# Performance work log

Hardware: AMD Instinct MI355X
Metric: run time of the kernel (lower is better)

The kernel has to match this reference:

```python
import jax, jax.numpy as jnp
import numpy as np

N, M, C, CSKIP, K = 16384, 4096, 256, 128, 3
BIG = 1e10  # distance penalty for cross-batch pairs


def setup_inputs() -> dict:
    key = jax.random.key(0)
    ks = jax.random.split(key, 6)
    return {
        "x": jax.random.normal(ks[0], (M, C), jnp.float32),
        "pos": jax.random.normal(ks[1], (M, 3), jnp.float32),
        "batch": jnp.zeros((M,), jnp.int32),
        "x_skip": jax.random.normal(ks[2], (N, CSKIP), jnp.float32),
        "pos_skip": jax.random.normal(ks[3], (N, 3), jnp.float32),
        "batch_skip": jnp.zeros((N,), jnp.int32),
        "W1": jax.random.normal(ks[4], (C + CSKIP, 256), jnp.float32) * (1.0 / np.sqrt(C + CSKIP)),
        "b1": jnp.zeros((256,), jnp.float32),
        "W2": jax.random.normal(ks[5], (256, 256), jnp.float32) * (1.0 / np.sqrt(256)),
        "b2": jnp.zeros((256,), jnp.float32),
    }


def _knn_idx(pos, pos_skip, batch, batch_skip, k):
    # Squared distances via GEMM form: [N, M]
    a2 = jnp.sum(pos_skip * pos_skip, axis=-1, keepdims=True)      # [N,1]
    b2 = jnp.sum(pos * pos, axis=-1)[None, :]                       # [1,M]
    d2 = a2 + b2 - 2.0 * (pos_skip @ pos.T)                         # [N,M]
    d2 = jnp.where(batch_skip[:, None] != batch[None, :], BIG, d2)
    _, idx = jax.lax.top_k(-d2, k)                                  # [N,k]
    return idx


def reference(x, pos, batch, x_skip, pos_skip, batch_skip, W1, b1, W2, b2):
    idx = _knn_idx(pos, pos_skip, batch, batch_skip, K)             # [N,k] coarse neighbor ids
    # Exact squared dist recomputed from gathered positions (matches torch diff path)
    diff = pos_skip[:, None, :] - pos[idx]                          # [N,k,3]
    d2 = jnp.sum(diff * diff, axis=-1, keepdims=True)               # [N,k,1]
    w = 1.0 / (d2 + 1e-8)                                           # inverse-distance weights
    wsum = jnp.sum(w, axis=1, keepdims=True)                        # per-row scatter_add == sum over k
    w = w / (wsum + 1e-8)
    x_interp = jnp.sum(w * x[idx], axis=1)                          # [N,C]
    h = jnp.concatenate([x_interp, x_skip], axis=1)                 # [N,C+C']
    h = jax.nn.relu(h @ W1 + b1)
    h = jax.nn.relu(h @ W2 + b2)
    return h
```

## Files before the change

### kernel.cpp

```cpp
#include <hip/hip_runtime.h>

typedef float     f4   __attribute__((ext_vector_type(4)));
typedef float     f32x4 __attribute__((ext_vector_type(4)));
typedef _Float16  h8   __attribute__((ext_vector_type(8)));
typedef _Float16  h4   __attribute__((ext_vector_type(4)));
typedef _Float16  h2   __attribute__((ext_vector_type(2)));

#define NQ   16384
#define MP   4096
#define CF   256
#define CSK  128
#define K1   384
#define HID  256
#define QBK  64

__device__ __forceinline__ unsigned umed3(unsigned a, unsigned b, unsigned c) {
    unsigned r;
    asm("v_med3_u32 %0, %1, %2, %3" : "=v"(r) : "v"(a), "v"(b), "v"(c));
    return r;
}

__global__ __launch_bounds__(256) void wconv_kernel(
    const float* __restrict__ W1, const float* __restrict__ W2,
    _Float16* __restrict__ Wt1, _Float16* __restrict__ Wt2)
{
    const int i = blockIdx.x * 256 + threadIdx.x;
    if (i < K1 * HID) {
        const int k = i >> 8, n = i & 255;
        Wt1[(size_t)(k >> 5) * 8192 + ((k >> 3) & 3) * 2048 + n * 8 + (k & 7)]
            = (_Float16)W1[i];
    } else {
        const int i2 = i - K1 * HID;
        const int k = i2 >> 8, n = i2 & 255;
        Wt2[(size_t)(k >> 5) * 8192 + ((k >> 3) & 3) * 2048 + n * 8 + (k & 7)]
            = (_Float16)W2[i2];
    }
}

__global__ __launch_bounds__(512, 2) void fused_kernel(
    const float* __restrict__ pos,
    const float* __restrict__ pos_skip,
    const float* __restrict__ x,
    const float* __restrict__ x_skip,
    const _Float16* __restrict__ Wt1,
    const _Float16* __restrict__ Wt2,
    const float* __restrict__ b1,
    const float* __restrict__ b2,
    float* __restrict__ out)
{
    __shared__ __align__(16) char smem[51712];
    _Float16* pxh = (_Float16*)smem;
    _Float16* pyh = (_Float16*)(smem + 8192);
    _Float16* pzh = (_Float16*)(smem + 16384);
    unsigned short (*ci)[48] = (unsigned short (*)[48])(smem + 24576);
    _Float16 (*As)[392] = (_Float16 (*)[392])smem;
    _Float16 (*Hs)[264] = (_Float16 (*)[264])smem;
    int   (*fidx)[3] = (int (*)[3])(smem + 50176);
    float (*fw)[3]   = (float (*)[3])(smem + 50944);

    const int tid = threadIdx.x;

    {
        const f4* posv = (const f4*)pos;
        for (int m = tid; m < MP / 4; m += 512) {
            const f4 a = posv[3*m], b = posv[3*m+1], c = posv[3*m+2];
            h4 hx, hy, hz;
            hx[0]=(_Float16)a[0]; hx[1]=(_Float16)a[3];
            hx[2]=(_Float16)b[2]; hx[3]=(_Float16)c[1];
            hy[0]=(_Float16)a[1]; hy[1]=(_Float16)b[0];
            hy[2]=(_Float16)b[3]; hy[3]=(_Float16)c[2];
            hz[0]=(_Float16)a[2]; hz[1]=(_Float16)b[1];
            hz[2]=(_Float16)c[0]; hz[3]=(_Float16)c[3];
            *(h4*)&pxh[4*m] = hx;
            *(h4*)&pyh[4*m] = hy;
            *(h4*)&pzh[4*m] = hz;
        }
    }
    __syncthreads();

    const int lane = tid & 63;
    const int wv   = tid >> 6;

    {
        h2 q2x[8], q2y[8], q2z[8];
        #pragma unroll
        for (int k = 0; k < 8; k++) {
            const int q = blockIdx.x * QBK + wv * 8 + k;
            const _Float16 hx = (_Float16)pos_skip[3*q+0];
            const _Float16 hy = (_Float16)pos_skip[3*q+1];
            const _Float16 hz = (_Float16)pos_skip[3*q+2];
            q2x[k][0] = hx; q2x[k][1] = hx;
            q2y[k][0] = hy; q2y[k][1] = hy;
            q2z[k][0] = hz; q2z[k][1] = hz;
        }

        unsigned K0[8], K1v[8], K2[8];
        #pragma unroll
        for (int k = 0; k < 8; k++) { K0[k] = ~0u; K1v[k] = ~0u; K2[k] = ~0u; }

        #define INS(k, key) {                                              \
            const unsigned o0 = K0[k], o1 = K1v[k], o2 = K2[k];            \
            K0[k]  = min(o0, (key));                                       \
            K1v[k] = umed3(o0, o1, (key));                                 \
            K2[k]  = umed3(o1, o2, (key));                                 \
        }

        union hpack { h4 v4; h2 v2[2]; };
        #define EVALP(CX, CY, CZ, JB)                                      \
            _Pragma("unroll")                                              \
            for (int k = 0; k < 8; k++) {                                  \
                _Pragma("unroll")                                          \
                for (int pp = 0; pp < 2; pp++) {                           \
                    const h2 dx = q2x[k] - (CX).v2[pp];                    \
                    const h2 dy = q2y[k] - (CY).v2[pp];                    \
                    const h2 dz = q2z[k] - (CZ).v2[pp];                    \
                    const h2 dd = dx*dx + dy*dy + dz*dz;                   \
                    const unsigned du = __builtin_bit_cast(unsigned, dd);  \
                    const unsigned key0 = ((du & 0xFFFFu) << 12) + (JB) + pp*2; \
                    const unsigned key1 = ((du >> 16) << 12) + (JB) + pp*2 + 1; \
                    INS(k, key0);                                          \
                    INS(k, key1);                                          \
                }                                                          \
            }

        const h4* px4 = (const h4*)pxh;
        const h4* py4 = (const h4*)pyh;
        const h4* pz4 = (const h4*)pzh;

        hpack cx, cy, cz, nx, ny, nz;
        int idx = lane;
        cx.v4 = px4[idx]; cy.v4 = py4[idx]; cz.v4 = pz4[idx];

        for (int it = 0; it < 16; ++it) {
            const int nidx = idx + 64;
            nx.v4 = px4[nidx]; ny.v4 = py4[nidx]; nz.v4 = pz4[nidx];
            const unsigned jb = (unsigned)(it * 256 + lane * 4);
            EVALP(cx, cy, cz, jb);
            cx = nx; cy = ny; cz = nz;
            idx = nidx;
        }
        #undef EVALP
        #undef INS

        #pragma unroll
        for (int k = 0; k < 8; k++) {
            unsigned a0 = K0[k], a1 = K1v[k], a2 = K2[k];
            {
                const unsigned b0 = (unsigned)__builtin_amdgcn_ds_swizzle((int)a0, 0x041F);
                const unsigned b1 = (unsigned)__builtin_amdgcn_ds_swizzle((int)a1, 0x041F);
                const unsigned b2 = (unsigned)__builtin_amdgcn_ds_swizzle((int)a2, 0x041F);
                const unsigned m0 = min(a0, b0);
                const unsigned c1 = max(a0, b0);
                const unsigned d0 = min(a1, b1), d1 = max(a1, b1);
                const unsigned m1 = min(c1, d0);
                const unsigned m2 = min(min(max(c1, d0), d1), min(a2, b2));
                a0 = m0; a1 = m1; a2 = m2;
            }
            {
                const unsigned b0 = (unsigned)__builtin_amdgcn_ds_swizzle((int)a0, 0x081F);
                const unsigned b1 = (unsigned)__builtin_amdgcn_ds_swizzle((int)a1, 0x081F);
                const unsigned b2 = (unsigned)__builtin_amdgcn_ds_swizzle((int)a2, 0x081F);
                const unsigned m0 = min(a0, b0);
                const unsigned c1 = max(a0, b0);
                const unsigned d0 = min(a1, b1), d1 = max(a1, b1);
                const unsigned m1 = min(c1, d0);
                const unsigned m2 = min(min(max(c1, d0), d1), min(a2, b2));
                a0 = m0; a1 = m1; a2 = m2;
            }
            if (!(lane & 3)) {
                const int q = wv * 8 + k;
                const int pr = lane >> 2;
                ci[q][pr*3+0] = (unsigned short)(a0 & 0xFFFu);
                ci[q][pr*3+1] = (unsigned short)(a1 & 0xFFFu);
                ci[q][pr*3+2] = (unsigned short)(a2 & 0xFFFu);
            }
        }
    }
    __syncthreads();

    {
        const int q    = tid >> 3;
        const int part = tid & 7;
        const int g    = blockIdx.x * QBK + q;
        const double qxd = (double)pos_skip[3*g+0];
        const double qyd = (double)pos_skip[3*g+1];
        const double qzd = (double)pos_skip[3*g+2];
        const double a2d = qxd*qxd + qyd*qyd + qzd*qzd;

        double e0 = 1e300, e1 = 1e300, e2 = 1e300;
        int    j0 = 0,     j1 = 0,     j2 = 0;
        #pragma unroll
        for (int c = 0; c < 6; c++) {
            const int j = ci[q][part*6 + c];
            const double pxd = (double)pos[3*j+0];
            const double pyd = (double)pos[3*j+1];
            const double pzd = (double)pos[3*j+2];
            const double b2  = pxd*pxd + pyd*pyd + pzd*pzd;
            const double dot = qxd*pxd + qyd*pyd + qzd*pzd;
            const double d   = (a2d + b2) - 2.0 * dot;
            if (d < e2) {
                if (d < e1) {
                    e2 = e1; j2 = j1;
                    if (d < e0) { e1 = e0; j1 = j0; e0 = d; j0 = j; }
                    else        { e1 = d;  j1 = j; }
                } else { e2 = d; j2 = j; }
            }
        }
        ci[q][part*3+0] = (unsigned short)j0;
        ci[q][part*3+1] = (unsigned short)j1;
        ci[q][part*3+2] = (unsigned short)j2;
    }
    __syncthreads();

    if (tid < QBK) {
        const int g = blockIdx.x * QBK + tid;
        const double qxd = (double)pos_skip[3*g+0];
        const double qyd = (double)pos_skip[3*g+1];
        const double qzd = (double)pos_skip[3*g+2];
        const double a2d = qxd*qxd + qyd*qyd + qzd*qzd;

        double e0 = 1e300, e1 = 1e300, e2 = 1e300;
        int    j0 = 0,     j1 = 0,     j2 = 0;
        for (int p = 0; p < 8; p++) {
            #pragma unroll
            for (int s = 0; s < 3; s++) {
                const int j = ci[tid][p*3+s];
                const double pxd = (double)pos[3*j+0];
                const double pyd = (double)pos[3*j+1];
                const double pzd = (double)pos[3*j+2];
                const double b2  = pxd*pxd + pyd*pyd + pzd*pzd;
                const double dot = qxd*pxd + qyd*pyd + qzd*pzd;
                const double d   = (a2d + b2) - 2.0 * dot;
                if (d < e2) {
                    if (d < e1) {
                        e2 = e1; j2 = j1;
                        if (d < e0) { e1 = e0; j1 = j0; e0 = d; j0 = j; }
                        else        { e1 = d;  j1 = j; }
                    } else { e2 = d; j2 = j; }
                }
            }
        }
        const float sx = pos_skip[3*g+0], sy = pos_skip[3*g+1], sz = pos_skip[3*g+2];
        const int jj[3] = { j0, j1, j2 };
        float wv3[3];
        #pragma unroll
        for (int k = 0; k < 3; k++) {
            const float dx = sx - pos[3*jj[k]+0];
            const float dy = sy - pos[3*jj[k]+1];
            const float dz = sz - pos[3*jj[k]+2];
            const float dd = dx*dx + dy*dy + dz*dz;
            wv3[k] = 1.0f / (dd + 1e-8f);
        }
        const float inv = 1.0f / (wv3[0] + wv3[1] + wv3[2] + 1e-8f);
        #pragma unroll
        for (int k = 0; k < 3; k++) {
            fidx[tid][k] = jj[k];
            fw[tid][k]   = wv3[k] * inv;
        }
    }
    __syncthreads();

    const int row0 = blockIdx.x * QBK;

    {
        const int r   = tid >> 3;
        const int sub = tid & 7;
        const int g   = row0 + r;
        const int j0 = fidx[r][0], j1 = fidx[r][1], j2 = fidx[r][2];
        const float w0 = fw[r][0], w1 = fw[r][1], w2 = fw[r][2];
        const f4* xa = (const f4*)(x + (size_t)j0 * CF);
        const f4* xb = (const f4*)(x + (size_t)j1 * CF);
        const f4* xc = (const f4*)(x + (size_t)j2 * CF);
        const f4* xs = (const f4*)(x_skip + (size_t)g * CSK);
        #pragma unroll
        for (int t = 0; t < 8; t++) {
            const int c4 = t * 8 + sub;
            const f4 a = xa[c4], b = xb[c4], c = xc[c4];
            const f4 v = a * w0 + b * w1 + c * w2;
            h4 hv; hv[0]=(_Float16)v[0]; hv[1]=(_Float16)v[1];
                   hv[2]=(_Float16)v[2]; hv[3]=(_Float16)v[3];
            *(h4*)&As[r][c4 * 4] = hv;
        }
        #pragma unroll
        for (int t = 0; t < 4; t++) {
            const int c4 = t * 8 + sub;
            const f4 v = xs[c4];
            h4 hv; hv[0]=(_Float16)v[0]; hv[1]=(_Float16)v[1];
                   hv[2]=(_Float16)v[2]; hv[3]=(_Float16)v[3];
            *(h4*)&As[r][CF + c4 * 4] = hv;
        }
    }

    const int ln   = tid & 15;
    const int quad = (tid >> 4) & 3;
    const int nb   = wv * 32;
    const int q8   = quad * 8;

    const _Float16* w1b = Wt1 + quad * 2048 + (size_t)(nb + ln) * 8;
    const _Float16* w2b = Wt2 + quad * 2048 + (size_t)(nb + ln) * 8;

    f32x4 acc[4][2];
    #pragma unroll
    for (int rg = 0; rg < 4; rg++)
        #pragma unroll
        for (int nt = 0; nt < 2; nt++) acc[rg][nt] = (f32x4)0.0f;

    h8 B[2][2];
    #pragma unroll
    for (int s = 0; s < 2; s++)
        #pragma unroll
        for (int nt = 0; nt < 2; nt++)
            B[s][nt] = *(const h8*)(w1b + (size_t)s * 8192 + nt * 128);

    __syncthreads();

    #pragma unroll
    for (int kb = 0; kb < 12; kb++) {
        const int s = kb & 1;
        h8 hb[2];
        #pragma unroll
        for (int nt = 0; nt < 2; nt++) hb[nt] = B[s][nt];
        const int nk = kb + 2;
        if (nk < 12) {
            #pragma unroll
            for (int nt = 0; nt < 2; nt++)
                B[s][nt] = *(const h8*)(w1b + (size_t)nk * 8192 + nt * 128);
        } else {
            #pragma unroll
            for (int nt = 0; nt < 2; nt++)
                B[s][nt] = *(const h8*)(w2b + (size_t)(nk - 12) * 8192 + nt * 128);
        }
        #pragma unroll
        for (int rg = 0; rg < 4; rg++) {
            const h8 ha = *(const h8*)&As[rg * 16 + ln][kb * 32 + q8];
            #pragma unroll
            for (int nt = 0; nt < 2; nt++)
                acc[rg][nt] = __builtin_amdgcn_mfma_f32_16x16x32_f16(ha, hb[nt], acc[rg][nt], 0, 0, 0);
        }
    }
    __syncthreads();

    #pragma unroll
    for (int nt = 0; nt < 2; nt++) {
        const int n = nb + nt * 16 + ln;
        const float bv = b1[n];
        #pragma unroll
        for (int rg = 0; rg < 4; rg++) {
            #pragma unroll
            for (int r = 0; r < 4; r++) {
                Hs[rg * 16 + quad * 4 + r][n] =
                    (_Float16)fmaxf(acc[rg][nt][r] + bv, 0.0f);
            }
            acc[rg][nt] = (f32x4)0.0f;
        }
    }
    __syncthreads();

    #pragma unroll
    for (int kb = 0; kb < 8; kb++) {
        const int s = kb & 1;
        h8 hb[2];
        #pragma unroll
        for (int nt = 0; nt < 2; nt++) hb[nt] = B[s][nt];
        const int nk = kb + 2;
        if (nk < 8) {
            #pragma unroll
            for (int nt = 0; nt < 2; nt++)
                B[s][nt] = *(const h8*)(w2b + (size_t)nk * 8192 + nt * 128);
        }
        #pragma unroll
        for (int rg = 0; rg < 4; rg++) {
            const h8 ha = *(const h8*)&Hs[rg * 16 + ln][kb * 32 + q8];
            #pragma unroll
            for (int nt = 0; nt < 2; nt++)
                acc[rg][nt] = __builtin_amdgcn_mfma_f32_16x16x32_f16(ha, hb[nt], acc[rg][nt], 0, 0, 0);
        }
    }

    #pragma unroll
    for (int nt = 0; nt < 2; nt++) {
        const int n = nb + nt * 16 + ln;
        const float bv = b2[n];
        #pragma unroll
        for (int rg = 0; rg < 4; rg++) {
            #pragma unroll
            for (int r = 0; r < 4; r++) {
                const int m = rg * 16 + quad * 4 + r;
                out[(size_t)(row0 + m) * HID + n] = fmaxf(acc[rg][nt][r] + bv, 0.0f);
            }
        }
    }
}

extern "C" void kernel_launch(void* const* d_in, const int* in_sizes, int n_in,
                              void* d_out, int out_size, void* d_ws, size_t ws_size,
                              hipStream_t stream) {
    const float* x         = (const float*)d_in[0];
    const float* pos       = (const float*)d_in[1];
    const float* x_skip    = (const float*)d_in[3];
    const float* pos_skip  = (const float*)d_in[4];
    const float* W1        = (const float*)d_in[6];
    const float* b1        = (const float*)d_in[7];
    const float* W2        = (const float*)d_in[8];
    const float* b2        = (const float*)d_in[9];
    float* out = (float*)d_out;

    char* ws = (char*)d_ws;
    _Float16* Wt1 = (_Float16*)ws;
    _Float16* Wt2 = (_Float16*)(ws + 196608);

    wconv_kernel<<<(K1*HID + HID*HID) / 256, 256, 0, stream>>>(W1, W2, Wt1, Wt2);
    fused_kernel<<<NQ / QBK, 512, 0, stream>>>(pos, pos_skip, x, x_skip,
                                               Wt1, Wt2, b1, b2, out);
}
```

Before: 123.6 us.

## Batch neighbor position loads and deepen weight prefetch, relax launch bounds

```diff
diff --git a/kernel.cpp b/kernel.cpp
--- a/kernel.cpp
+++ b/kernel.cpp
@@ -37,7 +37,7 @@
     }
 }
 
-__global__ __launch_bounds__(512, 2) void fused_kernel(
+__global__ __launch_bounds__(512, 1) void fused_kernel(
     const float* __restrict__ pos,
     const float* __restrict__ pos_skip,
     const float* __restrict__ x,
@@ -182,6 +182,18 @@
         const int q    = tid >> 3;
         const int part = tid & 7;
         const int g    = blockIdx.x * QBK + q;
+
+        int jarr[6];
+        #pragma unroll
+        for (int c = 0; c < 6; c++) jarr[c] = ci[q][part*6 + c];
+        float pxf[6], pyf[6], pzf[6];
+        #pragma unroll
+        for (int c = 0; c < 6; c++) {
+            pxf[c] = pos[3*jarr[c]+0];
+            pyf[c] = pos[3*jarr[c]+1];
+            pzf[c] = pos[3*jarr[c]+2];
+        }
+
         const double qxd = (double)pos_skip[3*g+0];
         const double qyd = (double)pos_skip[3*g+1];
         const double qzd = (double)pos_skip[3*g+2];
@@ -191,10 +203,10 @@
         int    j0 = 0,     j1 = 0,     j2 = 0;
         #pragma unroll
         for (int c = 0; c < 6; c++) {
-            const int j = ci[q][part*6 + c];
-            const double pxd = (double)pos[3*j+0];
-            const double pyd = (double)pos[3*j+1];
-            const double pzd = (double)pos[3*j+2];
+            const int j = jarr[c];
+            const double pxd = (double)pxf[c];
+            const double pyd = (double)pyf[c];
+            const double pzd = (double)pzf[c];
             const double b2  = pxd*pxd + pyd*pyd + pzd*pzd;
             const double dot = qxd*pxd + qyd*pyd + qzd*pzd;
             const double d   = (a2d + b2) - 2.0 * dot;
@@ -214,6 +226,18 @@
 
     if (tid < QBK) {
         const int g = blockIdx.x * QBK + tid;
+
+        int jarr[24];
+        #pragma unroll
+        for (int c = 0; c < 24; c++) jarr[c] = ci[tid][c];
+        float pxf[24], pyf[24], pzf[24];
+        #pragma unroll
+        for (int c = 0; c < 24; c++) {
+            pxf[c] = pos[3*jarr[c]+0];
+            pyf[c] = pos[3*jarr[c]+1];
+            pzf[c] = pos[3*jarr[c]+2];
+        }
+
         const double qxd = (double)pos_skip[3*g+0];
         const double qyd = (double)pos_skip[3*g+1];
         const double qzd = (double)pos_skip[3*g+2];
@@ -221,23 +245,21 @@
 
         double e0 = 1e300, e1 = 1e300, e2 = 1e300;
         int    j0 = 0,     j1 = 0,     j2 = 0;
-        for (int p = 0; p < 8; p++) {
-            #pragma unroll
-            for (int s = 0; s < 3; s++) {
-                const int j = ci[tid][p*3+s];
-                const double pxd = (double)pos[3*j+0];
-                const double pyd = (double)pos[3*j+1];
-                const double pzd = (double)pos[3*j+2];
-                const double b2  = pxd*pxd + pyd*pyd + pzd*pzd;
-                const double dot = qxd*pxd + qyd*pyd + qzd*pzd;
-                const double d   = (a2d + b2) - 2.0 * dot;
-                if (d < e2) {
-                    if (d < e1) {
-                        e2 = e1; j2 = j1;
-                        if (d < e0) { e1 = e0; j1 = j0; e0 = d; j0 = j; }
-                        else        { e1 = d;  j1 = j; }
-                    } else { e2 = d; j2 = j; }
-                }
+        #pragma unroll
+        for (int c = 0; c < 24; c++) {
+            const int j = jarr[c];
+            const double pxd = (double)pxf[c];
+            const double pyd = (double)pyf[c];
+            const double pzd = (double)pzf[c];
+            const double b2  = pxd*pxd + pyd*pyd + pzd*pzd;
+            const double dot = qxd*pxd + qyd*pyd + qzd*pzd;
+            const double d   = (a2d + b2) - 2.0 * dot;
+            if (d < e2) {
+                if (d < e1) {
+                    e2 = e1; j2 = j1;
+                    if (d < e0) { e1 = e0; j1 = j0; e0 = d; j0 = j; }
+                    else        { e1 = d;  j1 = j; }
+                } else { e2 = d; j2 = j; }
             }
         }
         const float sx = pos_skip[3*g+0], sy = pos_skip[3*g+1], sz = pos_skip[3*g+2];
@@ -305,9 +327,9 @@
         #pragma unroll
         for (int nt = 0; nt < 2; nt++) acc[rg][nt] = (f32x4)0.0f;
 
-    h8 B[2][2];
-    #pragma unroll
-    for (int s = 0; s < 2; s++)
+    h8 B[4][2];
+    #pragma unroll
+    for (int s = 0; s < 4; s++)
         #pragma unroll
         for (int nt = 0; nt < 2; nt++)
             B[s][nt] = *(const h8*)(w1b + (size_t)s * 8192 + nt * 128);
@@ -316,11 +338,11 @@
 
     #pragma unroll
     for (int kb = 0; kb < 12; kb++) {
-        const int s = kb & 1;
+        const int s = kb & 3;
         h8 hb[2];
         #pragma unroll
         for (int nt = 0; nt < 2; nt++) hb[nt] = B[s][nt];
-        const int nk = kb + 2;
+        const int nk = kb + 4;
         if (nk < 12) {
             #pragma unroll
             for (int nt = 0; nt < 2; nt++)
@@ -358,11 +380,11 @@
 
     #pragma unroll
     for (int kb = 0; kb < 8; kb++) {
-        const int s = kb & 1;
+        const int s = kb & 3;
         h8 hb[2];
         #pragma unroll
         for (int nt = 0; nt < 2; nt++) hb[nt] = B[s][nt];
-        const int nk = kb + 2;
+        const int nk = kb + 4;
         if (nk < 8) {
             #pragma unroll
             for (int nt = 0; nt < 2; nt++)
```

After: 120.8 us. 1.02x faster.
